# Performance work log

Hardware: AMD Instinct MI355X
Metric: run time of the kernel (lower is better)

The kernel has to match this reference:

```python
import jax, jax.numpy as jnp
import numpy as np

N_NODES = 100000
N_EDGES = 1600000
IN_DIM = 128
HEADS = 4
OUT_C = 32
NEG_SLOPE = 0.2


def setup_inputs() -> dict:
    key = jax.random.key(0)
    ks = jax.random.split(key, 8)
    x = jax.random.normal(ks[0], (N_NODES, IN_DIM), dtype=jnp.float32)
    # glorot-ish scale for linear weights
    s = float(np.sqrt(2.0 / (IN_DIM + HEADS * OUT_C)))
    W_l = jax.random.normal(ks[1], (IN_DIM, HEADS * OUT_C), dtype=jnp.float32) * s
    b_l = jnp.zeros((HEADS * OUT_C,), dtype=jnp.float32)
    W_r = jax.random.normal(ks[2], (IN_DIM, HEADS * OUT_C), dtype=jnp.float32) * s
    b_r = jnp.zeros((HEADS * OUT_C,), dtype=jnp.float32)
    att = jax.random.normal(ks[3], (HEADS, OUT_C), dtype=jnp.float32) * float(np.sqrt(2.0 / (HEADS + OUT_C)))
    bias = jnp.zeros((HEADS * OUT_C,), dtype=jnp.float32)
    src = jax.random.randint(ks[4], (N_EDGES,), 0, N_NODES, dtype=jnp.int64)
    dst = jax.random.randint(ks[5], (N_EDGES,), 0, N_NODES, dtype=jnp.int64)
    # remove accidental self loops (the module strips them before re-adding)
    dst = jnp.where(dst == src, (dst + 1) % N_NODES, dst)
    return {"x": x, "W_l": W_l, "b_l": b_l, "W_r": W_r, "b_r": b_r,
            "att": att, "bias": bias, "src": src, "dst": dst}


def reference(x, W_l, b_l, W_r, b_r, att, bias, src, dst):
    N = x.shape[0]
    H, C = att.shape
    # linear transforms: source (lin_l) and target (lin_r) projections
    x_l = (x @ W_l + b_l).reshape(N, H, C)
    x_r = (x @ W_r + b_r).reshape(N, H, C)
    # add self loops (static shape)
    loop = jnp.arange(N, dtype=src.dtype)
    s = jnp.concatenate([src, loop])
    d = jnp.concatenate([dst, loop])
    # per-edge GATv2 score: a^T LeakyReLU(Theta_l x_j + Theta_r x_i)
    m = x_l[s] + x_r[d]                       # [E+N, H, C]
    m = jnp.where(m >= 0, m, NEG_SLOPE * m)   # LeakyReLU
    e = jnp.einsum('ehc,hc->eh', m, att)      # [E+N, H]
    # scatter-softmax over incoming edges of each destination node
    seg_max = jax.ops.segment_max(e, d, num_segments=N)   # [N, H]
    e = jnp.exp(e - seg_max[d])
    denom = jax.ops.segment_sum(e, d, num_segments=N)     # [N, H]
    alpha = e / denom[d]                                   # every node has a self loop -> denom > 0
    # weighted scatter-add of source messages
    out = jax.ops.segment_sum(alpha[:, :, None] * x_l[s], d, num_segments=N)  # [N, H, C]
    return out.reshape(N, H * C) + bias
```

## Files before the change

### kernel.cpp

```cpp
#include <hip/hip_runtime.h>
#include <hip/hip_bf16.h>
#include <cstdint>

#define N_NODES 100000
#define N_EDGES 1600000
#define DIM 128
#define GR 32
#define GEMM_BLOCKS (N_NODES / GR)
#define HIST_BLOCKS ((N_EDGES + 255) / 256)

__device__ __forceinline__ float lr(float v) { return fmaxf(v, 0.2f * v); }

__global__ __launch_bounds__(256) void gemm_hist(
    const float* __restrict__ x,
    const float* __restrict__ Wl, const float* __restrict__ bl,
    const float* __restrict__ Wr, const float* __restrict__ br,
    float* __restrict__ xl, float* __restrict__ xr,
    const int* __restrict__ dst, int* __restrict__ deg) {
  __shared__ float xs[GR][DIM];
  const int tid = threadIdx.x;

  if (blockIdx.x >= GEMM_BLOCKS) {
    const int i = (blockIdx.x - GEMM_BLOCKS) * 256 + tid;
    if (i < N_EDGES) atomicAdd(&deg[dst[i]], 1);
    return;
  }

  const int row0 = blockIdx.x * GR;

#pragma unroll
  for (int i = 0; i < 4; ++i) {
    const int idx = i * 256 + tid;
    const int r = idx >> 5;
    const int c4 = idx & 31;
    const float4 v = *reinterpret_cast<const float4*>(
        x + (size_t)(row0 + r) * DIM + c4 * 4);
    *reinterpret_cast<float4*>(&xs[r][c4 * 4]) = v;
  }
  __syncthreads();

  const int cg = tid & 63;
  const int rg = tid >> 6;
  const int which = cg >> 5;
  const int col0 = (cg & 31) * 4;
  const float* __restrict__ W = which ? Wr : Wl;
  const float* __restrict__ b = which ? br : bl;
  float* __restrict__ o = which ? xr : xl;
  const int r0 = rg * 8;

  float acc[8][4];
#pragma unroll
  for (int r = 0; r < 8; ++r)
#pragma unroll
    for (int c = 0; c < 4; ++c) acc[r][c] = 0.f;

  for (int kb = 0; kb < DIM; kb += 4) {
    float4 w0 = *reinterpret_cast<const float4*>(W + (kb + 0) * DIM + col0);
    float4 w1 = *reinterpret_cast<const float4*>(W + (kb + 1) * DIM + col0);
    float4 w2 = *reinterpret_cast<const float4*>(W + (kb + 2) * DIM + col0);
    float4 w3 = *reinterpret_cast<const float4*>(W + (kb + 3) * DIM + col0);
#pragma unroll
    for (int r = 0; r < 8; ++r) {
      const float4 xv = *reinterpret_cast<const float4*>(&xs[r0 + r][kb]);
      acc[r][0] = fmaf(xv.x, w0.x, acc[r][0]);
      acc[r][1] = fmaf(xv.x, w0.y, acc[r][1]);
      acc[r][2] = fmaf(xv.x, w0.z, acc[r][2]);
      acc[r][3] = fmaf(xv.x, w0.w, acc[r][3]);
      acc[r][0] = fmaf(xv.y, w1.x, acc[r][0]);
      acc[r][1] = fmaf(xv.y, w1.y, acc[r][1]);
      acc[r][2] = fmaf(xv.y, w1.z, acc[r][2]);
      acc[r][3] = fmaf(xv.y, w1.w, acc[r][3]);
      acc[r][0] = fmaf(xv.z, w2.x, acc[r][0]);
      acc[r][1] = fmaf(xv.z, w2.y, acc[r][1]);
      acc[r][2] = fmaf(xv.z, w2.z, acc[r][2]);
      acc[r][3] = fmaf(xv.z, w2.w, acc[r][3]);
      acc[r][0] = fmaf(xv.w, w3.x, acc[r][0]);
      acc[r][1] = fmaf(xv.w, w3.y, acc[r][1]);
      acc[r][2] = fmaf(xv.w, w3.z, acc[r][2]);
      acc[r][3] = fmaf(xv.w, w3.w, acc[r][3]);
    }
  }

  const float4 bb = *reinterpret_cast<const float4*>(b + col0);
#pragma unroll
  for (int r = 0; r < 8; ++r) {
    float4 ov;
    ov.x = acc[r][0] + bb.x;
    ov.y = acc[r][1] + bb.y;
    ov.z = acc[r][2] + bb.z;
    ov.w = acc[r][3] + bb.w;
    *reinterpret_cast<float4*>(o + (size_t)(row0 + r0 + r) * DIM + col0) = ov;
  }
}

__global__ __launch_bounds__(1024) void scan1(const int* __restrict__ deg,
                                              int* __restrict__ excl,
                                              int* __restrict__ bsum) {
  __shared__ int tmp[1024];
  const int tid = threadIdx.x;
  const int gid = blockIdx.x * 1024 + tid;
  const int v = (gid < N_NODES) ? deg[gid] : 0;
  int xacc = v;
  tmp[tid] = v;
  __syncthreads();
  for (int offd = 1; offd < 1024; offd <<= 1) {
    const int t = (tid >= offd) ? tmp[tid - offd] : 0;
    __syncthreads();
    xacc += t;
    tmp[tid] = xacc;
    __syncthreads();
  }
  if (gid < N_NODES) excl[gid] = xacc - v;
  if (tid == 1023) bsum[blockIdx.x] = xacc;
}

__global__ __launch_bounds__(128) void scan2(int* __restrict__ bsum, int nb) {
  __shared__ int tmp[128];
  const int tid = threadIdx.x;
  const int v = (tid < nb) ? bsum[tid] : 0;
  int xacc = v;
  tmp[tid] = v;
  __syncthreads();
  for (int offd = 1; offd < 128; offd <<= 1) {
    const int t = (tid >= offd) ? tmp[tid - offd] : 0;
    __syncthreads();
    xacc += t;
    tmp[tid] = xacc;
    __syncthreads();
  }
  if (tid < nb) bsum[tid] = xacc - v;
}

__global__ __launch_bounds__(1024) void scan3(int* __restrict__ offs,
                                              const int* __restrict__ bsum,
                                              int* __restrict__ fill) {
  const int gid = blockIdx.x * 1024 + threadIdx.x;
  if (gid < N_NODES) {
    const int o = offs[gid] + bsum[blockIdx.x];
    offs[gid] = o;
    fill[gid] = o;
  }
  if (gid == N_NODES) offs[N_NODES] = N_EDGES;
}

__global__ __launch_bounds__(256) void scatter_kernel(const int* __restrict__ src,
                                                      const int* __restrict__ dst,
                                                      int* __restrict__ fill,
                                                      int* __restrict__ csr) {
  const int i = blockIdx.x * 256 + threadIdx.x;
  if (i < N_EDGES) {
    const int slot = atomicAdd(&fill[dst[i]], 1);
    csr[slot] = src[i];
  }
}

__global__ __launch_bounds__(256) void gat_node(
    const float* __restrict__ xl,
    const float* __restrict__ att, const float* __restrict__ bias,
    const int* __restrict__ offs, const int* __restrict__ csr,
    float* __restrict__ out) {
  const int wid = (blockIdx.x * 256 + threadIdx.x) >> 6;
  const int lane = threadIdx.x & 63;
  if (wid >= N_NODES) return;
  const int d = wid;
  const int q = lane >> 4;
  const int i = lane & 15;
  const int c0 = i * 8;

  const float4 aA = *reinterpret_cast<const float4*>(att + c0);
  const float4 aB = *reinterpret_cast<const float4*>(att + c0 + 4);
  const float4 rA = *reinterpret_cast<const float4*>(out + (size_t)d * DIM + c0);
  const float4 rB = *reinterpret_cast<const float4*>(out + (size_t)d * DIM + c0 + 4);
  const float4 sA = *reinterpret_cast<const float4*>(xl + (size_t)d * DIM + c0);
  const float4 sB = *reinterpret_cast<const float4*>(xl + (size_t)d * DIM + c0 + 4);

  float p = lr(sA.x + rA.x) * aA.x + lr(sA.y + rA.y) * aA.y
          + lr(sA.z + rA.z) * aA.z + lr(sA.w + rA.w) * aA.w
          + lr(sB.x + rB.x) * aB.x + lr(sB.y + rB.y) * aB.y
          + lr(sB.z + rB.z) * aB.z + lr(sB.w + rB.w) * aB.w;
  p += __shfl_xor(p, 1);
  p += __shfl_xor(p, 2);

  const bool q0 = (q == 0);
  float m = q0 ? p : -1e30f;
  float l = q0 ? 1.f : 0.f;
  float4 cA, cB;
  cA.x = q0 ? sA.x : 0.f;  cA.y = q0 ? sA.y : 0.f;
  cA.z = q0 ? sA.z : 0.f;  cA.w = q0 ? sA.w : 0.f;
  cB.x = q0 ? sB.x : 0.f;  cB.y = q0 ? sB.y : 0.f;
  cB.z = q0 ? sB.z : 0.f;  cB.w = q0 ? sB.w : 0.f;

  const int beg = offs[d];
  const int end = offs[d + 1];

  for (int cbase = beg; cbase < end; cbase += 64) {
    const int idx = cbase + lane;
    const int sv = csr[idx < end ? idx : end - 1];
    const int cnt = min(64, end - cbase);
    const int nj = (cnt + 3) >> 2;

    const int s0 = __shfl(sv, q);
    const float* rp0 = xl + (size_t)s0 * DIM + c0;
    float4 nA = *reinterpret_cast<const float4*>(rp0);
    float4 nB = *reinterpret_cast<const float4*>(rp0 + 4);

    for (int j = 0; j < nj; ++j) {
      const float4 xA = nA;
      const float4 xB = nB;
      if (j + 1 < nj) {
        const int s1 = __shfl(sv, 4 * (j + 1) + q);
        const float* rp = xl + (size_t)s1 * DIM + c0;
        nA = *reinterpret_cast<const float4*>(rp);
        nB = *reinterpret_cast<const float4*>(rp + 4);
      }
      const bool valid = (4 * j + q) < cnt;

      float ek = lr(xA.x + rA.x) * aA.x + lr(xA.y + rA.y) * aA.y
               + lr(xA.z + rA.z) * aA.z + lr(xA.w + rA.w) * aA.w
               + lr(xB.x + rB.x) * aB.x + lr(xB.y + rB.y) * aB.y
               + lr(xB.z + rB.z) * aB.z + lr(xB.w + rB.w) * aB.w;
      ek += __shfl_xor(ek, 1);
      ek += __shfl_xor(ek, 2);
      ek = valid ? ek : -2e30f;

      const float mn = fmaxf(m, ek);
      const float sc = __expf(m - mn);
      float w = __expf(ek - mn);
      w = valid ? w : 0.f;
      l = l * sc + w;
      cA.x = fmaf(cA.x, sc, w * xA.x);
      cA.y = fmaf(cA.y, sc, w * xA.y);
      cA.z = fmaf(cA.z, sc, w * xA.z);
      cA.w = fmaf(cA.w, sc, w * xA.w);
      cB.x = fmaf(cB.x, sc, w * xB.x);
      cB.y = fmaf(cB.y, sc, w * xB.y);
      cB.z = fmaf(cB.z, sc, w * xB.z);
      cB.w = fmaf(cB.w, sc, w * xB.w);
      m = mn;
    }
  }

  auto merge = [&](int mask) {
    const float mo = __shfl_xor(m, mask);
    const float lo = __shfl_xor(l, mask);
    float4 oA, oB;
    oA.x = __shfl_xor(cA.x, mask);  oA.y = __shfl_xor(cA.y, mask);
    oA.z = __shfl_xor(cA.z, mask);  oA.w = __shfl_xor(cA.w, mask);
    oB.x = __shfl_xor(cB.x, mask);  oB.y = __shfl_xor(cB.y, mask);
    oB.z = __shfl_xor(cB.z, mask);  oB.w = __shfl_xor(cB.w, mask);
    const float ms = fmaxf(m, mo);
    const float w1 = __expf(m - ms);
    const float w2 = __expf(mo - ms);
    l = l * w1 + lo * w2;
    cA.x = cA.x * w1 + oA.x * w2;  cA.y = cA.y * w1 + oA.y * w2;
    cA.z = cA.z * w1 + oA.z * w2;  cA.w = cA.w * w1 + oA.w * w2;
    cB.x = cB.x * w1 + oB.x * w2;  cB.y = cB.y * w1 + oB.y * w2;
    cB.z = cB.z * w1 + oB.z * w2;  cB.w = cB.w * w1 + oB.w * w2;
    m = ms;
  };
  merge(16);
  merge(32);

  if (lane < 16) {
    const float inv = 1.f / l;
    const float4 bA = *reinterpret_cast<const float4*>(bias + c0);
    const float4 bB = *reinterpret_cast<const float4*>(bias + c0 + 4);
    float4 oA, oB;
    oA.x = cA.x * inv + bA.x;  oA.y = cA.y * inv + bA.y;
    oA.z = cA.z * inv + bA.z;  oA.w = cA.w * inv + bA.w;
    oB.x = cB.x * inv + bB.x;  oB.y = cB.y * inv + bB.y;
    oB.z = cB.z * inv + bB.z;  oB.w = cB.w * inv + bB.w;
    *reinterpret_cast<float4*>(out + (size_t)d * DIM + c0) = oA;
    *reinterpret_cast<float4*>(out + (size_t)d * DIM + c0 + 4) = oB;
  }
}

extern "C" void kernel_launch(void* const* d_in, const int* in_sizes, int n_in,
                              void* d_out, int out_size, void* d_ws, size_t ws_size,
                              hipStream_t stream) {
  const float* x    = (const float*)d_in[0];
  const float* Wl   = (const float*)d_in[1];
  const float* bl   = (const float*)d_in[2];
  const float* Wr   = (const float*)d_in[3];
  const float* br   = (const float*)d_in[4];
  const float* att  = (const float*)d_in[5];
  const float* bias = (const float*)d_in[6];
  const int* src    = (const int*)d_in[7];
  const int* dst    = (const int*)d_in[8];
  float* out = (float*)d_out;

  char* w = (char*)d_ws;
  size_t off = 0;
  auto alloc = [&](size_t bytes) -> void* {
    void* p = w + off;
    off = (off + bytes + 255) & ~(size_t)255;
    return p;
  };
  float* xl = (float*)alloc((size_t)N_NODES * DIM * 4);
  int* deg  = (int*)alloc((size_t)N_NODES * 4);
  int* offs = (int*)alloc((size_t)(N_NODES + 1) * 4);
  int* fill = (int*)alloc((size_t)N_NODES * 4);
  int* bsum = (int*)alloc(1024);
  int* csr  = (int*)alloc((size_t)N_EDGES * 4);
  float* xr = out;

  const int nscan_blocks = (N_NODES + 1023) / 1024;

  hipMemsetAsync(deg, 0, (size_t)N_NODES * 4, stream);
  gemm_hist<<<GEMM_BLOCKS + HIST_BLOCKS, 256, 0, stream>>>(
      x, Wl, bl, Wr, br, xl, xr, dst, deg);
  scan1<<<nscan_blocks, 1024, 0, stream>>>(deg, offs, bsum);
  scan2<<<1, 128, 0, stream>>>(bsum, nscan_blocks);
  scan3<<<nscan_blocks, 1024, 0, stream>>>(offs, bsum, fill);
  scatter_kernel<<<(N_EDGES + 255) / 256, 256, 0, stream>>>(src, dst, fill, csr);
  gat_node<<<(N_NODES * 64 + 255) / 256, 256, 0, stream>>>(xl, att, bias, offs, csr, out);
}
```

Before: 487.8 us.

## Drop scan3 kernel, vectorize histogram/scatter, prefetch weights in GEMM

Removes the scan3 pass by having the scatter kernel add block sums on the fly and by deriving segment bounds in gat_node from loc+bsum and deg. The histogram and scatter now read dst/src as int4 with four atomics per thread, and the histogram uses a fixed grid-stride count of blocks. The GEMM inner loop software-prefetches the next weight rows. This saves one launch and some memory traffic, but adds an extra bsum lookup per edge and depends on the edge count being divisible by four.

```diff
diff --git a/kernel.cpp b/kernel.cpp
--- a/kernel.cpp
+++ b/kernel.cpp
@@ -7,7 +7,7 @@
 #define DIM 128
 #define GR 32
 #define GEMM_BLOCKS (N_NODES / GR)
-#define HIST_BLOCKS ((N_EDGES + 255) / 256)
+#define HIST_BLOCKS 512
 
 __device__ __forceinline__ float lr(float v) { return fmaxf(v, 0.2f * v); }
 
@@ -21,8 +21,16 @@
   const int tid = threadIdx.x;
 
   if (blockIdx.x >= GEMM_BLOCKS) {
-    const int i = (blockIdx.x - GEMM_BLOCKS) * 256 + tid;
-    if (i < N_EDGES) atomicAdd(&deg[dst[i]], 1);
+    const int4* __restrict__ dst4 = reinterpret_cast<const int4*>(dst);
+    const int stride = HIST_BLOCKS * 256;
+    for (int i = (blockIdx.x - GEMM_BLOCKS) * 256 + tid;
+         i < N_EDGES / 4; i += stride) {
+      const int4 d4 = dst4[i];
+      atomicAdd(&deg[d4.x], 1);
+      atomicAdd(&deg[d4.y], 1);
+      atomicAdd(&deg[d4.z], 1);
+      atomicAdd(&deg[d4.w], 1);
+    }
     return;
   }
 
@@ -54,31 +62,39 @@
 #pragma unroll
     for (int c = 0; c < 4; ++c) acc[r][c] = 0.f;
 
+  float4 wa0 = *reinterpret_cast<const float4*>(W + 0 * DIM + col0);
+  float4 wa1 = *reinterpret_cast<const float4*>(W + 1 * DIM + col0);
+  float4 wa2 = *reinterpret_cast<const float4*>(W + 2 * DIM + col0);
+  float4 wa3 = *reinterpret_cast<const float4*>(W + 3 * DIM + col0);
+
+#pragma unroll 4
   for (int kb = 0; kb < DIM; kb += 4) {
-    float4 w0 = *reinterpret_cast<const float4*>(W + (kb + 0) * DIM + col0);
-    float4 w1 = *reinterpret_cast<const float4*>(W + (kb + 1) * DIM + col0);
-    float4 w2 = *reinterpret_cast<const float4*>(W + (kb + 2) * DIM + col0);
-    float4 w3 = *reinterpret_cast<const float4*>(W + (kb + 3) * DIM + col0);
+    const int kn = (kb + 4 < DIM) ? kb + 4 : kb;
+    const float4 wb0 = *reinterpret_cast<const float4*>(W + (kn + 0) * DIM + col0);
+    const float4 wb1 = *reinterpret_cast<const float4*>(W + (kn + 1) * DIM + col0);
+    const float4 wb2 = *reinterpret_cast<const float4*>(W + (kn + 2) * DIM + col0);
+    const float4 wb3 = *reinterpret_cast<const float4*>(W + (kn + 3) * DIM + col0);
 #pragma unroll
     for (int r = 0; r < 8; ++r) {
       const float4 xv = *reinterpret_cast<const float4*>(&xs[r0 + r][kb]);
-      acc[r][0] = fmaf(xv.x, w0.x, acc[r][0]);
-      acc[r][1] = fmaf(xv.x, w0.y, acc[r][1]);
-      acc[r][2] = fmaf(xv.x, w0.z, acc[r][2]);
-      acc[r][3] = fmaf(xv.x, w0.w, acc[r][3]);
-      acc[r][0] = fmaf(xv.y, w1.x, acc[r][0]);
-      acc[r][1] = fmaf(xv.y, w1.y, acc[r][1]);
-      acc[r][2] = fmaf(xv.y, w1.z, acc[r][2]);
-      acc[r][3] = fmaf(xv.y, w1.w, acc[r][3]);
-      acc[r][0] = fmaf(xv.z, w2.x, acc[r][0]);
-      acc[r][1] = fmaf(xv.z, w2.y, acc[r][1]);
-      acc[r][2] = fmaf(xv.z, w2.z, acc[r][2]);
-      acc[r][3] = fmaf(xv.z, w2.w, acc[r][3]);
-      acc[r][0] = fmaf(xv.w, w3.x, acc[r][0]);
-      acc[r][1] = fmaf(xv.w, w3.y, acc[r][1]);
-      acc[r][2] = fmaf(xv.w, w3.z, acc[r][2]);
-      acc[r][3] = fmaf(xv.w, w3.w, acc[r][3]);
+      acc[r][0] = fmaf(xv.x, wa0.x, acc[r][0]);
+      acc[r][1] = fmaf(xv.x, wa0.y, acc[r][1]);
+      acc[r][2] = fmaf(xv.x, wa0.z, acc[r][2]);
+      acc[r][3] = fmaf(xv.x, wa0.w, acc[r][3]);
+      acc[r][0] = fmaf(xv.y, wa1.x, acc[r][0]);
+      acc[r][1] = fmaf(xv.y, wa1.y, acc[r][1]);
+      acc[r][2] = fmaf(xv.y, wa1.z, acc[r][2]);
+      acc[r][3] = fmaf(xv.y, wa1.w, acc[r][3]);
+      acc[r][0] = fmaf(xv.z, wa2.x, acc[r][0]);
+      acc[r][1] = fmaf(xv.z, wa2.y, acc[r][1]);
+      acc[r][2] = fmaf(xv.z, wa2.z, acc[r][2]);
+      acc[r][3] = fmaf(xv.z, wa2.w, acc[r][3]);
+      acc[r][0] = fmaf(xv.w, wa3.x, acc[r][0]);
+      acc[r][1] = fmaf(xv.w, wa3.y, acc[r][1]);
+      acc[r][2] = fmaf(xv.w, wa3.z, acc[r][2]);
+      acc[r][3] = fmaf(xv.w, wa3.w, acc[r][3]);
     }
+    wa0 = wb0; wa1 = wb1; wa2 = wb2; wa3 = wb3;
   }
 
   const float4 bb = *reinterpret_cast<const float4*>(b + col0);
@@ -94,7 +110,7 @@
 }
 
 __global__ __launch_bounds__(1024) void scan1(const int* __restrict__ deg,
-                                              int* __restrict__ excl,
+                                              int* __restrict__ loc,
                                               int* __restrict__ bsum) {
   __shared__ int tmp[1024];
   const int tid = threadIdx.x;
@@ -110,7 +126,7 @@
     tmp[tid] = xacc;
     __syncthreads();
   }
-  if (gid < N_NODES) excl[gid] = xacc - v;
+  if (gid < N_NODES) loc[gid] = xacc - v;
   if (tid == 1023) bsum[blockIdx.x] = xacc;
 }
 
@@ -131,33 +147,30 @@
   if (tid < nb) bsum[tid] = xacc - v;
 }
 
-__global__ __launch_bounds__(1024) void scan3(int* __restrict__ offs,
-                                              const int* __restrict__ bsum,
-                                              int* __restrict__ fill) {
-  const int gid = blockIdx.x * 1024 + threadIdx.x;
-  if (gid < N_NODES) {
-    const int o = offs[gid] + bsum[blockIdx.x];
-    offs[gid] = o;
-    fill[gid] = o;
-  }
-  if (gid == N_NODES) offs[N_NODES] = N_EDGES;
-}
-
 __global__ __launch_bounds__(256) void scatter_kernel(const int* __restrict__ src,
                                                       const int* __restrict__ dst,
-                                                      int* __restrict__ fill,
+                                                      int* __restrict__ loc,
+                                                      const int* __restrict__ bsum,
                                                       int* __restrict__ csr) {
+  const int4* __restrict__ src4 = reinterpret_cast<const int4*>(src);
+  const int4* __restrict__ dst4 = reinterpret_cast<const int4*>(dst);
   const int i = blockIdx.x * 256 + threadIdx.x;
-  if (i < N_EDGES) {
-    const int slot = atomicAdd(&fill[dst[i]], 1);
-    csr[slot] = src[i];
+  if (i < N_EDGES / 4) {
+    const int4 s4 = src4[i];
+    const int4 d4 = dst4[i];
+    int slot;
+    slot = atomicAdd(&loc[d4.x], 1) + bsum[d4.x >> 10];  csr[slot] = s4.x;
+    slot = atomicAdd(&loc[d4.y], 1) + bsum[d4.y >> 10];  csr[slot] = s4.y;
+    slot = atomicAdd(&loc[d4.z], 1) + bsum[d4.z >> 10];  csr[slot] = s4.z;
+    slot = atomicAdd(&loc[d4.w], 1) + bsum[d4.w >> 10];  csr[slot] = s4.w;
   }
 }
 
 __global__ __launch_bounds__(256) void gat_node(
     const float* __restrict__ xl,
     const float* __restrict__ att, const float* __restrict__ bias,
-    const int* __restrict__ offs, const int* __restrict__ csr,
+    const int* __restrict__ loc, const int* __restrict__ deg,
+    const int* __restrict__ bsum, const int* __restrict__ csr,
     float* __restrict__ out) {
   const int wid = (blockIdx.x * 256 + threadIdx.x) >> 6;
   const int lane = threadIdx.x & 63;
@@ -190,8 +203,9 @@
   cB.x = q0 ? sB.x : 0.f;  cB.y = q0 ? sB.y : 0.f;
   cB.z = q0 ? sB.z : 0.f;  cB.w = q0 ? sB.w : 0.f;
 
-  const int beg = offs[d];
-  const int end = offs[d + 1];
+  const int dg = deg[d];
+  const int end = loc[d] + bsum[d >> 10];
+  const int beg = end - dg;
 
   for (int cbase = beg; cbase < end; cbase += 64) {
     const int idx = cbase + lane;
@@ -298,8 +312,7 @@
   };
   float* xl = (float*)alloc((size_t)N_NODES * DIM * 4);
   int* deg  = (int*)alloc((size_t)N_NODES * 4);
-  int* offs = (int*)alloc((size_t)(N_NODES + 1) * 4);
-  int* fill = (int*)alloc((size_t)N_NODES * 4);
+  int* loc  = (int*)alloc((size_t)N_NODES * 4);
   int* bsum = (int*)alloc(1024);
   int* csr  = (int*)alloc((size_t)N_EDGES * 4);
   float* xr = out;
@@ -309,9 +322,10 @@
   hipMemsetAsync(deg, 0, (size_t)N_NODES * 4, stream);
   gemm_hist<<<GEMM_BLOCKS + HIST_BLOCKS, 256, 0, stream>>>(
       x, Wl, bl, Wr, br, xl, xr, dst, deg);
-  scan1<<<nscan_blocks, 1024, 0, stream>>>(deg, offs, bsum);
+  scan1<<<nscan_blocks, 1024, 0, stream>>>(deg, loc, bsum);
   scan2<<<1, 128, 0, stream>>>(bsum, nscan_blocks);
-  scan3<<<nscan_blocks, 1024, 0, stream>>>(offs, bsum, fill);
-  scatter_kernel<<<(N_EDGES + 255) / 256, 256, 0, stream>>>(src, dst, fill, csr);
-  gat_node<<<(N_NODES * 64 + 255) / 256, 256, 0, stream>>>(xl, att, bias, offs, csr, out);
-}
+  scatter_kernel<<<(N_EDGES / 4 + 255) / 256, 256, 0, stream>>>(
+      src, dst, loc, bsum, csr);
+  gat_node<<<(N_NODES * 64 + 255) / 256, 256, 0, stream>>>(
+      xl, att, bias, loc, deg, bsum, csr, out);
+}
```

Measured after the change: 499.1 us. +2.3%, slower.

## Drop scan3 pass, vectorize scatter, and enlarge GEMM row tile

Applied to the files above, without the earlier changes.

Removes the scan3 kernel: scatter now adds the block prefix sum to a per-block local offset counter it increments atomically, and gat_node recovers the segment range as end minus degree. The scatter kernel reads src and dst as int4 and processes four edges per thread. The GEMM tile grows from 32 to 64 rows per block (16 rows per thread), with bounds guards. The aim is to save one kernel launch and a pass over offsets, cut scatter thread count, and reuse weights more in the GEMM, at the cost of more accumulator registers and an extra bsum read per edge.

```diff
diff --git a/kernel.cpp b/kernel.cpp
--- a/kernel.cpp
+++ b/kernel.cpp
@@ -5,8 +5,8 @@
 #define N_NODES 100000
 #define N_EDGES 1600000
 #define DIM 128
-#define GR 32
-#define GEMM_BLOCKS (N_NODES / GR)
+#define GR 64
+#define GEMM_BLOCKS ((N_NODES + GR - 1) / GR)
 #define HIST_BLOCKS ((N_EDGES + 255) / 256)
 
 __device__ __forceinline__ float lr(float v) { return fmaxf(v, 0.2f * v); }
@@ -29,12 +29,13 @@
   const int row0 = blockIdx.x * GR;
 
 #pragma unroll
-  for (int i = 0; i < 4; ++i) {
+  for (int i = 0; i < 8; ++i) {
     const int idx = i * 256 + tid;
     const int r = idx >> 5;
     const int c4 = idx & 31;
+    const int rr = min(row0 + r, N_NODES - 1);
     const float4 v = *reinterpret_cast<const float4*>(
-        x + (size_t)(row0 + r) * DIM + c4 * 4);
+        x + (size_t)rr * DIM + c4 * 4);
     *reinterpret_cast<float4*>(&xs[r][c4 * 4]) = v;
   }
   __syncthreads();
@@ -46,21 +47,21 @@
   const float* __restrict__ W = which ? Wr : Wl;
   const float* __restrict__ b = which ? br : bl;
   float* __restrict__ o = which ? xr : xl;
-  const int r0 = rg * 8;
-
-  float acc[8][4];
-#pragma unroll
-  for (int r = 0; r < 8; ++r)
+  const int r0 = rg * 16;
+
+  float acc[16][4];
+#pragma unroll
+  for (int r = 0; r < 16; ++r)
 #pragma unroll
     for (int c = 0; c < 4; ++c) acc[r][c] = 0.f;
 
   for (int kb = 0; kb < DIM; kb += 4) {
-    float4 w0 = *reinterpret_cast<const float4*>(W + (kb + 0) * DIM + col0);
-    float4 w1 = *reinterpret_cast<const float4*>(W + (kb + 1) * DIM + col0);
-    float4 w2 = *reinterpret_cast<const float4*>(W + (kb + 2) * DIM + col0);
-    float4 w3 = *reinterpret_cast<const float4*>(W + (kb + 3) * DIM + col0);
-#pragma unroll
-    for (int r = 0; r < 8; ++r) {
+    const float4 w0 = *reinterpret_cast<const float4*>(W + (kb + 0) * DIM + col0);
+    const float4 w1 = *reinterpret_cast<const float4*>(W + (kb + 1) * DIM + col0);
+    const float4 w2 = *reinterpret_cast<const float4*>(W + (kb + 2) * DIM + col0);
+    const float4 w3 = *reinterpret_cast<const float4*>(W + (kb + 3) * DIM + col0);
+#pragma unroll
+    for (int r = 0; r < 16; ++r) {
       const float4 xv = *reinterpret_cast<const float4*>(&xs[r0 + r][kb]);
       acc[r][0] = fmaf(xv.x, w0.x, acc[r][0]);
       acc[r][1] = fmaf(xv.x, w0.y, acc[r][1]);
@@ -83,18 +84,21 @@
 
   const float4 bb = *reinterpret_cast<const float4*>(b + col0);
 #pragma unroll
-  for (int r = 0; r < 8; ++r) {
-    float4 ov;
-    ov.x = acc[r][0] + bb.x;
-    ov.y = acc[r][1] + bb.y;
-    ov.z = acc[r][2] + bb.z;
-    ov.w = acc[r][3] + bb.w;
-    *reinterpret_cast<float4*>(o + (size_t)(row0 + r0 + r) * DIM + col0) = ov;
+  for (int r = 0; r < 16; ++r) {
+    const int row = row0 + r0 + r;
+    if (row < N_NODES) {
+      float4 ov;
+      ov.x = acc[r][0] + bb.x;
+      ov.y = acc[r][1] + bb.y;
+      ov.z = acc[r][2] + bb.z;
+      ov.w = acc[r][3] + bb.w;
+      *reinterpret_cast<float4*>(o + (size_t)row * DIM + col0) = ov;
+    }
   }
 }
 
 __global__ __launch_bounds__(1024) void scan1(const int* __restrict__ deg,
-                                              int* __restrict__ excl,
+                                              int* __restrict__ loc,
                                               int* __restrict__ bsum) {
   __shared__ int tmp[1024];
   const int tid = threadIdx.x;
@@ -110,7 +114,7 @@
     tmp[tid] = xacc;
     __syncthreads();
   }
-  if (gid < N_NODES) excl[gid] = xacc - v;
+  if (gid < N_NODES) loc[gid] = xacc - v;
   if (tid == 1023) bsum[blockIdx.x] = xacc;
 }
 
@@ -131,33 +135,30 @@
   if (tid < nb) bsum[tid] = xacc - v;
 }
 
-__global__ __launch_bounds__(1024) void scan3(int* __restrict__ offs,
-                                              const int* __restrict__ bsum,
-                                              int* __restrict__ fill) {
-  const int gid = blockIdx.x * 1024 + threadIdx.x;
-  if (gid < N_NODES) {
-    const int o = offs[gid] + bsum[blockIdx.x];
-    offs[gid] = o;
-    fill[gid] = o;
-  }
-  if (gid == N_NODES) offs[N_NODES] = N_EDGES;
-}
-
 __global__ __launch_bounds__(256) void scatter_kernel(const int* __restrict__ src,
                                                       const int* __restrict__ dst,
-                                                      int* __restrict__ fill,
+                                                      int* __restrict__ loc,
+                                                      const int* __restrict__ bsum,
                                                       int* __restrict__ csr) {
+  const int4* __restrict__ src4 = reinterpret_cast<const int4*>(src);
+  const int4* __restrict__ dst4 = reinterpret_cast<const int4*>(dst);
   const int i = blockIdx.x * 256 + threadIdx.x;
-  if (i < N_EDGES) {
-    const int slot = atomicAdd(&fill[dst[i]], 1);
-    csr[slot] = src[i];
+  if (i < N_EDGES / 4) {
+    const int4 s4 = src4[i];
+    const int4 d4 = dst4[i];
+    int slot;
+    slot = atomicAdd(&loc[d4.x], 1) + bsum[d4.x >> 10];  csr[slot] = s4.x;
+    slot = atomicAdd(&loc[d4.y], 1) + bsum[d4.y >> 10];  csr[slot] = s4.y;
+    slot = atomicAdd(&loc[d4.z], 1) + bsum[d4.z >> 10];  csr[slot] = s4.z;
+    slot = atomicAdd(&loc[d4.w], 1) + bsum[d4.w >> 10];  csr[slot] = s4.w;
   }
 }
 
 __global__ __launch_bounds__(256) void gat_node(
     const float* __restrict__ xl,
     const float* __restrict__ att, const float* __restrict__ bias,
-    const int* __restrict__ offs, const int* __restrict__ csr,
+    const int* __restrict__ loc, const int* __restrict__ deg,
+    const int* __restrict__ bsum, const int* __restrict__ csr,
     float* __restrict__ out) {
   const int wid = (blockIdx.x * 256 + threadIdx.x) >> 6;
   const int lane = threadIdx.x & 63;
@@ -190,8 +191,9 @@
   cB.x = q0 ? sB.x : 0.f;  cB.y = q0 ? sB.y : 0.f;
   cB.z = q0 ? sB.z : 0.f;  cB.w = q0 ? sB.w : 0.f;
 
-  const int beg = offs[d];
-  const int end = offs[d + 1];
+  const int dg = deg[d];
+  const int end = loc[d] + bsum[d >> 10];
+  const int beg = end - dg;
 
   for (int cbase = beg; cbase < end; cbase += 64) {
     const int idx = cbase + lane;
@@ -298,8 +300,7 @@
   };
   float* xl = (float*)alloc((size_t)N_NODES * DIM * 4);
   int* deg  = (int*)alloc((size_t)N_NODES * 4);
-  int* offs = (int*)alloc((size_t)(N_NODES + 1) * 4);
-  int* fill = (int*)alloc((size_t)N_NODES * 4);
+  int* loc  = (int*)alloc((size_t)N_NODES * 4);
   int* bsum = (int*)alloc(1024);
   int* csr  = (int*)alloc((size_t)N_EDGES * 4);
   float* xr = out;
@@ -309,9 +310,10 @@
   hipMemsetAsync(deg, 0, (size_t)N_NODES * 4, stream);
   gemm_hist<<<GEMM_BLOCKS + HIST_BLOCKS, 256, 0, stream>>>(
       x, Wl, bl, Wr, br, xl, xr, dst, deg);
-  scan1<<<nscan_blocks, 1024, 0, stream>>>(deg, offs, bsum);
+  scan1<<<nscan_blocks, 1024, 0, stream>>>(deg, loc, bsum);
   scan2<<<1, 128, 0, stream>>>(bsum, nscan_blocks);
-  scan3<<<nscan_blocks, 1024, 0, stream>>>(offs, bsum, fill);
-  scatter_kernel<<<(N_EDGES + 255) / 256, 256, 0, stream>>>(src, dst, fill, csr);
-  gat_node<<<(N_NODES * 64 + 255) / 256, 256, 0, stream>>>(xl, att, bias, offs, csr, out);
-}
+  scatter_kernel<<<(N_EDGES / 4 + 255) / 256, 256, 0, stream>>>(
+      src, dst, loc, bsum, csr);
+  gat_node<<<(N_NODES * 64 + 255) / 256, 256, 0, stream>>>(
+      xl, att, bias, loc, deg, bsum, csr, out);
+}
```

Measured after the change: 491.7 us. Within noise of the previous version (+0.8%).
